# Optimization experiments

Measured on AMD Instinct MI355X. Metric: run time of the kernel, lower is better.

Reference implementation:

```python
import jax, jax.numpy as jnp
import numpy as np

NORM = float(1.0 / np.sqrt(2.0))


def haar1d_fwd(x):
    # forward 1D Haar along last axis; n must be a power of 2
    n = x.shape[-1]
    m = int(np.log2(n))
    length = n
    for _ in range(m):
        t = x[..., :length]
        e, o = t[..., ::2], t[..., 1::2]
        x = jnp.concatenate([NORM * (e + o), NORM * (e - o), x[..., length:]], axis=-1)
        length //= 2
    return x


def haar1d_inv(x):
    n = x.shape[-1]
    m = int(np.log2(n))
    length = 2
    for _ in range(m):
        half = length // 2
        a, d = x[..., :half], x[..., half:length]
        # interleave (a+d)/sqrt2 and (a-d)/sqrt2
        inter = jnp.stack([NORM * (a + d), NORM * (a - d)], axis=-1)
        inter = inter.reshape(x.shape[:-1] + (length,))
        x = jnp.concatenate([inter, x[..., length:]], axis=-1)
        length *= 2
    return x


def haar2d(x, inverse=False):
    f = haar1d_inv if inverse else haar1d_fwd
    x = f(x)                                        # along width
    x = jnp.swapaxes(f(jnp.swapaxes(x, -1, -2)), -1, -2)  # along height
    return x


def setup_inputs() -> dict:
    key = jax.random.key(0)
    k1, k2, k3, k4 = jax.random.split(key, 4)
    B, C, H, W, P = 16, 64, 256, 256, 2
    x = jax.random.normal(k1, (B, C, H, W), dtype=jnp.float32)
    v = jax.random.uniform(k2, (P, 1, 1, H, W), dtype=jnp.float32)
    conv_w = jax.random.normal(k3, (P, C, C), dtype=jnp.float32) * 0.05  # (pod, out_c, in_c)
    tau = jax.random.uniform(k4, (P, 1, 1, H, W), dtype=jnp.float32)
    return {"x": x, "v": v, "conv_w": conv_w, "tau": tau}


def reference(x, v, conv_w, tau):
    # H=W=256 are powers of 2 -> find_min_power padding is a no-op
    f1 = haar2d(x)  # forward 2D Haar
    acc = jnp.zeros_like(f1[:, :conv_w.shape[1]])
    for i in range(v.shape[0]):  # loop over pods (small, fixed)
        f3 = f1 * v[i]                                  # per-pixel spectral gate
        f4 = jnp.einsum('bchw,oc->bohw', f3, conv_w[i])  # 1x1 conv, no bias
        f5 = jnp.sign(f4) * jax.nn.relu(jnp.abs(f4) - tau[i])  # soft threshold
        acc = acc + f5
    y = haar2d(acc, inverse=True)
    return y + x  # residual
```

## Files before the change

kernel.cpp:

```cpp
#include <hip/hip_runtime.h>
#include <hip/hip_bf16.h>


namespace {

constexpr float kNorm = 0.70710678118654752440f;

typedef __attribute__((ext_vector_type(8))) short short8;
typedef __attribute__((ext_vector_type(4))) float f32x4;
typedef __attribute__((ext_vector_type(8))) unsigned short ushort8;
typedef __attribute__((ext_vector_type(4))) unsigned int uint4v;

__device__ __forceinline__ int ip2ref(int p) {
  if (p == 0) return 0;
  const int j = __builtin_ctz(p) + 1;
  return (256 >> j) + (p >> j);
}
__device__ __forceinline__ int ref2ip(int r) {
  if (r == 0) return 0;
  const int tb = 31 - __builtin_clz(r);
  const int j = 8 - tb;
  return ((r - (1 << tb)) << j) | (1 << (j - 1));
}

__device__ __forceinline__ unsigned short f2bf(float f) {
  unsigned int u = __float_as_uint(f);
  u += 0x7FFFu + ((u >> 16) & 1u);
  return (unsigned short)(u >> 16);
}
__device__ __forceinline__ float bf2f(unsigned int u) {
  return __uint_as_float((u & 0xFFFFu) << 16);
}
__device__ __forceinline__ unsigned pk2(float lo, float hi) {
  return (unsigned)f2bf(lo) | ((unsigned)f2bf(hi) << 16);
}

__device__ __forceinline__ void lift3f(const float f[8], float o[8]) {
  const float a0 = kNorm * (f[0] + f[1]), d10 = kNorm * (f[0] - f[1]);
  const float a1 = kNorm * (f[2] + f[3]), d11 = kNorm * (f[2] - f[3]);
  const float a2 = kNorm * (f[4] + f[5]), d12 = kNorm * (f[4] - f[5]);
  const float a3 = kNorm * (f[6] + f[7]), d13 = kNorm * (f[6] - f[7]);
  const float b0 = kNorm * (a0 + a1), d20 = kNorm * (a0 - a1);
  const float b1 = kNorm * (a2 + a3), d21 = kNorm * (a2 - a3);
  o[0] = kNorm * (b0 + b1);
  o[4] = kNorm * (b0 - b1);
  o[2] = d20; o[6] = d21;
  o[1] = d10; o[3] = d11; o[5] = d12; o[7] = d13;
}
__device__ __forceinline__ void ilift3f(const float f[8], float o[8]) {
  const float b0 = kNorm * (f[0] + f[4]), b1 = kNorm * (f[0] - f[4]);
  const float a0 = kNorm * (b0 + f[2]), a1 = kNorm * (b0 - f[2]);
  const float a2 = kNorm * (b1 + f[6]), a3 = kNorm * (b1 - f[6]);
  o[0] = kNorm * (a0 + f[1]); o[1] = kNorm * (a0 - f[1]);
  o[2] = kNorm * (a1 + f[3]); o[3] = kNorm * (a1 - f[3]);
  o[4] = kNorm * (a2 + f[5]); o[5] = kNorm * (a2 - f[5]);
  o[6] = kNorm * (a3 + f[7]); o[7] = kNorm * (a3 - f[7]);
}

__global__ __launch_bounds__(256) void k_prep(const float* __restrict__ cw,
                                              const float* __restrict__ vv,
                                              const float* __restrict__ tt,
                                              unsigned short* __restrict__ wb,
                                              unsigned int* __restrict__ vpk,
                                              unsigned int* __restrict__ tpk) {
  const int idx = blockIdx.x * 256 + threadIdx.x;
  if (idx < 8192) wb[idx] = f2bf(cw[idx]);
  const int w = idx >> 8;
  const int hp = idx & 255;
  const int off = (ip2ref(hp) << 8) + w;
  vpk[idx] = pk2(vv[off], vv[65536 + off]);
  tpk[idx] = pk2(tt[off], tt[65536 + off]);
}

__global__ __launch_bounds__(256) void k_fwdW(const float* __restrict__ x,
                                              unsigned short* __restrict__ xt) {
  __shared__ float tile[256][33];
  const int blk = blockIdx.x;
  const int img = blk >> 3;
  const int h0 = (blk & 7) << 5;
  const int tid = threadIdx.x;

  const float* __restrict__ src = x + ((size_t)img << 16) + ((size_t)h0 << 8);

  const int hR = tid >> 3;
  const int g = tid & 7;
#pragma unroll
  for (int it = 0; it < 4; ++it) {
    const int w0 = (g + (it << 3)) << 3;
    const float4 u = *reinterpret_cast<const float4*>(src + (hR << 8) + w0);
    const float4 v2 = *reinterpret_cast<const float4*>(src + (hR << 8) + w0 + 4);
    float f[8] = {u.x, u.y, u.z, u.w, v2.x, v2.y, v2.z, v2.w};
    float o[8];
    lift3f(f, o);
#pragma unroll
    for (int j = 0; j < 8; ++j) tile[w0 + j][hR] = o[j];
  }
  __syncthreads();

  if (tid < 128) {
    const int row = tid & 31;
    const int tq = tid >> 5;
    const int wq = tq << 6;
    float f[8], o[8];
#pragma unroll
    for (int j = 0; j < 8; ++j) f[j] = tile[wq + (j << 3)][row];
    lift3f(f, o);
#pragma unroll
    for (int j = 0; j < 8; ++j) tile[wq + (j << 3)][row] = o[j];
  }
  __syncthreads();

  if (tid < 32) {
    const float f0 = tile[0][tid], f1 = tile[64][tid];
    const float f2 = tile[128][tid], f3 = tile[192][tid];
    const float a0 = kNorm * (f0 + f1), d0 = kNorm * (f0 - f1);
    const float a1 = kNorm * (f2 + f3), d1 = kNorm * (f2 - f3);
    tile[0][tid] = kNorm * (a0 + a1);
    tile[64][tid] = d0;
    tile[128][tid] = kNorm * (a0 - a1);
    tile[192][tid] = d1;
  }
  __syncthreads();

  unsigned short* __restrict__ dst = xt + ((size_t)img << 16) + h0;
#pragma unroll
  for (int k = 0; k < 4; ++k) {
    const int idx = (k << 8) + tid;
    const int wp = idx >> 2;
    const int hseg = (idx & 3) << 3;
    const int wr = ip2ref(wp);
    ushort8 s;
#pragma unroll
    for (int j = 0; j < 8; ++j) s[j] = f2bf(tile[wp][hseg + j]);
    *reinterpret_cast<ushort8*>(dst + ((size_t)wr << 8) + hseg) = s;
  }
}

__device__ __forceinline__ int swzc(int h, int cdw) {
  return (h << 5) | ((cdw + ((h & 7) << 2) + (((h >> 3) & 3) << 3)) & 31);
}

__global__ __launch_bounds__(256, 3) void k_mid(
    unsigned short* __restrict__ ws, const unsigned short* __restrict__ wb,
    const unsigned int* __restrict__ vpk, const unsigned int* __restrict__ tpk) {
  __shared__ unsigned int t32[8192];
  __shared__ unsigned int vt[512];
  unsigned short* t16 = reinterpret_cast<unsigned short*>(t32);

  const int blk = blockIdx.x;
  const int b = blk >> 8;
  const int w = blk & 255;
  const int tid = threadIdx.x;

  unsigned short* __restrict__ base = ws + ((size_t)b << 22) + ((size_t)w << 8);

  vt[tid] = vpk[(w << 8) + tid];
  vt[256 + tid] = tpk[(w << 8) + tid];

  const int l15 = tid & 15;
  const int l4 = (tid & 63) >> 4;
  short8 Bf[4][4];
#pragma unroll
  for (int og = 0; og < 4; ++og) {
    const int o = (og << 4) + l15;
    const unsigned short* wr0 = wb + (o << 6) + (l4 << 3);
    const unsigned short* wr1 = wb + 4096 + (o << 6) + (l4 << 3);
    Bf[og][0] = *reinterpret_cast<const short8*>(wr0);
    Bf[og][1] = *reinterpret_cast<const short8*>(wr0 + 32);
    Bf[og][2] = *reinterpret_cast<const short8*>(wr1);
    Bf[og][3] = *reinterpret_cast<const short8*>(wr1 + 32);
  }

  const int cdw = tid >> 3;
  const int c0 = cdw << 1;
  const int o8 = tid & 7;
#pragma unroll
  for (int it = 0; it < 4; ++it) {
    const int h0 = (o8 << 3) + (it << 6);
    const ushort8 rA =
        *reinterpret_cast<const ushort8*>(base + ((size_t)c0 << 16) + h0);
    const ushort8 rB =
        *reinterpret_cast<const ushort8*>(base + ((size_t)(c0 + 1) << 16) + h0);
    float fa[8], fb[8], oa[8], ob[8];
#pragma unroll
    for (int j = 0; j < 8; ++j) {
      fa[j] = bf2f(rA[j]);
      fb[j] = bf2f(rB[j]);
    }
    lift3f(fa, oa);
    lift3f(fb, ob);
#pragma unroll
    for (int j = 0; j < 8; ++j) t32[swzc(h0 + j, cdw)] = pk2(oa[j], ob[j]);
  }
  __syncthreads();

  if (tid < 128) {
    const int cd = tid & 31;
    const int h0 = (tid >> 5) << 6;
    unsigned int g[8];
#pragma unroll
    for (int k = 0; k < 8; ++k) g[k] = t32[swzc(h0 + (k << 3), cd)];
    float fa[8], fb[8], oa[8], ob[8];
#pragma unroll
    for (int k = 0; k < 8; ++k) {
      fa[k] = bf2f(g[k]);
      fb[k] = bf2f(g[k] >> 16);
    }
    lift3f(fa, oa);
    lift3f(fb, ob);
#pragma unroll
    for (int k = 0; k < 8; ++k)
      t32[swzc(h0 + (k << 3), cd)] = pk2(oa[k], ob[k]);
  }
  __syncthreads();

  if (tid < 32) {
    unsigned int g[4];
#pragma unroll
    for (int k = 0; k < 4; ++k) g[k] = t32[swzc(k << 6, tid)];
    float fa[4], fb[4];
#pragma unroll
    for (int k = 0; k < 4; ++k) {
      fa[k] = bf2f(g[k]);
      fb[k] = bf2f(g[k] >> 16);
    }
    const float aa0 = kNorm * (fa[0] + fa[1]), da0 = kNorm * (fa[0] - fa[1]);
    const float aa1 = kNorm * (fa[2] + fa[3]), da1 = kNorm * (fa[2] - fa[3]);
    const float ab0 = kNorm * (fb[0] + fb[1]), db0 = kNorm * (fb[0] - fb[1]);
    const float ab1 = kNorm * (fb[2] + fb[3]), db1 = kNorm * (fb[2] - fb[3]);
    t32[swzc(0, tid)] = pk2(kNorm * (aa0 + aa1), kNorm * (ab0 + ab1));
    t32[swzc(64, tid)] = pk2(da0, db0);
    t32[swzc(128, tid)] = pk2(kNorm * (aa0 - aa1), kNorm * (ab0 - ab1));
    t32[swzc(192, tid)] = pk2(da1, db1);
  }
  __syncthreads();

  const int strip = (tid >> 6) << 6;
#pragma unroll 1
  for (int mt = 0; mt < 4; ++mt) {
    const int hh = strip + (mt << 4) + l15;
    const short8 a0 =
        *reinterpret_cast<const short8*>(&t32[swzc(hh, l4 << 2)]);
    const short8 a1 =
        *reinterpret_cast<const short8*>(&t32[swzc(hh, 16 + (l4 << 2))]);
    const int hb = strip + (mt << 4) + (l4 << 2);
    const uint4v vq = *reinterpret_cast<const uint4v*>(&vt[hb]);
    const uint4v tq = *reinterpret_cast<const uint4v*>(&vt[256 + hb]);
#pragma unroll
    for (int og = 0; og < 4; ++og) {
      const int o = (og << 4) + l15;
      f32x4 accL = {0.f, 0.f, 0.f, 0.f};
      f32x4 accH = {0.f, 0.f, 0.f, 0.f};
      accL = __builtin_amdgcn_mfma_f32_16x16x32_bf16(a0, Bf[og][0], accL, 0, 0, 0);
      accH = __builtin_amdgcn_mfma_f32_16x16x32_bf16(a0, Bf[og][2], accH, 0, 0, 0);
      accL = __builtin_amdgcn_mfma_f32_16x16x32_bf16(a1, Bf[og][1], accL, 0, 0, 0);
      accH = __builtin_amdgcn_mfma_f32_16x16x32_bf16(a1, Bf[og][3], accH, 0, 0, 0);
#pragma unroll
      for (int r = 0; r < 4; ++r) {
        const float v0 = bf2f(vq[r]), v1 = bf2f(vq[r] >> 16);
        const float t0 = bf2f(tq[r]), t1 = bf2f(tq[r] >> 16);
        const float g0 = accL[r] * v0;
        const float g1 = accH[r] * v1;
        float rr = 0.f;
        const float q0 = fabsf(g0) - t0;
        if (q0 > 0.f) rr += copysignf(q0, g0);
        const float q1 = fabsf(g1) - t1;
        if (q1 > 0.f) rr += copysignf(q1, g1);
        const int idx16 = (swzc(hb + r, o >> 1) << 1) | (o & 1);
        const float Fv = bf2f(t16[idx16]);
        t16[idx16] = f2bf(rr + Fv);
      }
    }
  }
  __syncthreads();

  if (tid < 32) {
    unsigned int g[4];
#pragma unroll
    for (int k = 0; k < 4; ++k) g[k] = t32[swzc(k << 6, tid)];
    float fa[4], fb[4];
#pragma unroll
    for (int k = 0; k < 4; ++k) {
      fa[k] = bf2f(g[k]);
      fb[k] = bf2f(g[k] >> 16);
    }
    const float ua0 = kNorm * (fa[0] + fa[2]), ua1 = kNorm * (fa[0] - fa[2]);
    const float ub0 = kNorm * (fb[0] + fb[2]), ub1 = kNorm * (fb[0] - fb[2]);
    t32[swzc(0, tid)] = pk2(kNorm * (ua0 + fa[1]), kNorm * (ub0 + fb[1]));
    t32[swzc(64, tid)] = pk2(kNorm * (ua0 - fa[1]), kNorm * (ub0 - fb[1]));
    t32[swzc(128, tid)] = pk2(kNorm * (ua1 + fa[3]), kNorm * (ub1 + fb[3]));
    t32[swzc(192, tid)] = pk2(kNorm * (ua1 - fa[3]), kNorm * (ub1 - fb[3]));
  }
  __syncthreads();

  if (tid < 128) {
    const int cd = tid & 31;
    const int h0 = (tid >> 5) << 6;
    unsigned int g[8];
#pragma unroll
    for (int k = 0; k < 8; ++k) g[k] = t32[swzc(h0 + (k << 3), cd)];
    float fa[8], fb[8], oa[8], ob[8];
#pragma unroll
    for (int k = 0; k < 8; ++k) {
      fa[k] = bf2f(g[k]);
      fb[k] = bf2f(g[k] >> 16);
    }
    ilift3f(fa, oa);
    ilift3f(fb, ob);
#pragma unroll
    for (int k = 0; k < 8; ++k)
      t32[swzc(h0 + (k << 3), cd)] = pk2(oa[k], ob[k]);
  }
  __syncthreads();

#pragma unroll
  for (int it = 0; it < 4; ++it) {
    const int h0 = (o8 << 3) + (it << 6);
    unsigned int g[8];
#pragma unroll
    for (int j = 0; j < 8; ++j) g[j] = t32[swzc(h0 + j, cdw)];
    float fa[8], fb[8], oa[8], ob[8];
#pragma unroll
    for (int j = 0; j < 8; ++j) {
      fa[j] = bf2f(g[j]);
      fb[j] = bf2f(g[j] >> 16);
    }
    ilift3f(fa, oa);
    ilift3f(fb, ob);
    ushort8 sA, sB;
#pragma unroll
    for (int j = 0; j < 8; ++j) {
      sA[j] = f2bf(oa[j]);
      sB[j] = f2bf(ob[j]);
    }
    *reinterpret_cast<ushort8*>(base + ((size_t)c0 << 16) + h0) = sA;
    *reinterpret_cast<ushort8*>(base + ((size_t)(c0 + 1) << 16) + h0) = sB;
  }
}

__global__ __launch_bounds__(256) void k_invW(const unsigned short* __restrict__ at,
                                              float* __restrict__ y) {
  __shared__ float tile[256][33];
  const int blk = blockIdx.x;
  const int img = blk >> 3;
  const int h0 = (blk & 7) << 5;
  const int tid = threadIdx.x;

  const unsigned short* __restrict__ basep = at + ((size_t)img << 16) + h0;
#pragma unroll
  for (int k = 0; k < 4; ++k) {
    const int idx = (k << 8) + tid;
    const int wp = idx >> 2;
    const int hseg = (idx & 3) << 3;
    const int wr = ip2ref(wp);
    const ushort8 rv =
        *reinterpret_cast<const ushort8*>(basep + ((size_t)wr << 8) + hseg);
#pragma unroll
    for (int j = 0; j < 8; ++j) tile[wp][hseg + j] = bf2f(rv[j]);
  }
  __syncthreads();

  if (tid < 32) {
    const float f0 = tile[0][tid], f1 = tile[64][tid];
    const float f2 = tile[128][tid], f3 = tile[192][tid];
    const float u0 = kNorm * (f0 + f2), u1 = kNorm * (f0 - f2);
    tile[0][tid] = kNorm * (u0 + f1);
    tile[64][tid] = kNorm * (u0 - f1);
    tile[128][tid] = kNorm * (u1 + f3);
    tile[192][tid] = kNorm * (u1 - f3);
  }
  __syncthreads();

  if (tid < 128) {
    const int row = tid & 31;
    const int tq = tid >> 5;
    const int wq = tq << 6;
    float f[8], o[8];
#pragma unroll
    for (int j = 0; j < 8; ++j) f[j] = tile[wq + (j << 3)][row];
    ilift3f(f, o);
#pragma unroll
    for (int j = 0; j < 8; ++j) tile[wq + (j << 3)][row] = o[j];
  }
  __syncthreads();

  const int hR = tid >> 3;
  const int g = tid & 7;
  float* __restrict__ yd = y + ((size_t)img << 16) + ((size_t)h0 << 8);
#pragma unroll
  for (int it = 0; it < 4; ++it) {
    const int w0 = (g + (it << 3)) << 3;
    float f[8], o[8];
#pragma unroll
    for (int j = 0; j < 8; ++j) f[j] = tile[w0 + j][hR];
    ilift3f(f, o);
    float4 y0 = {o[0], o[1], o[2], o[3]};
    float4 y1 = {o[4], o[5], o[6], o[7]};
    *reinterpret_cast<float4*>(yd + (hR << 8) + w0) = y0;
    *reinterpret_cast<float4*>(yd + (hR << 8) + w0 + 4) = y1;
  }
}

}

extern "C" void kernel_launch(void* const* d_in, const int* in_sizes, int n_in,
                              void* d_out, int out_size, void* d_ws, size_t ws_size,
                              hipStream_t stream) {
  (void)in_sizes; (void)n_in; (void)out_size; (void)ws_size;
  const float* x  = (const float*)d_in[0];
  const float* vv = (const float*)d_in[1];
  const float* cw = (const float*)d_in[2];
  const float* tt = (const float*)d_in[3];
  float* y = (float*)d_out;
  unsigned short* ws = (unsigned short*)d_ws;
  unsigned short* wb = ws + ((size_t)64 << 20);
  unsigned int* vpk = (unsigned int*)(ws + ((size_t)64 << 20) + 16384);
  unsigned int* tpk = vpk + 65536;

  k_prep<<<256, 256, 0, stream>>>(cw, vv, tt, wb, vpk, tpk);
  k_fwdW<<<8192, 256, 0, stream>>>(x, ws);
  k_mid <<<4096, 256, 0, stream>>>(ws, wb, vpk, tpk);
  k_invW<<<8192, 256, 0, stream>>>(ws, y);
}
```

Before: 261.6 us.

## Pack row pairs as bf16x2 in LDS for width Haar transforms

Reworks the forward and inverse width-direction Haar kernels so each LDS word holds two adjacent rows packed as bf16 pairs. The 256x33 fp32 tile becomes a 16x260 uint tile, so the transpose moves half as many bytes and uses vectorized 16-byte LDS accesses and rotated index orders to spread banks. This cuts LDS traffic and shared-memory footprint, which may allow more resident blocks. In exchange, intermediate lifting stages are rounded to bf16 inside the kernel instead of only at the output, which adds precision loss.

```diff
diff --git a/kernel.cpp b/kernel.cpp
--- a/kernel.cpp
+++ b/kernel.cpp
@@ -74,51 +74,80 @@
 
 __global__ __launch_bounds__(256) void k_fwdW(const float* __restrict__ x,
                                               unsigned short* __restrict__ xt) {
-  __shared__ float tile[256][33];
+  __shared__ unsigned int t[16][260];
   const int blk = blockIdx.x;
   const int img = blk >> 3;
   const int h0 = (blk & 7) << 5;
   const int tid = threadIdx.x;
 
   const float* __restrict__ src = x + ((size_t)img << 16) + ((size_t)h0 << 8);
-
-  const int hR = tid >> 3;
   const int g = tid & 7;
-#pragma unroll
-  for (int it = 0; it < 4; ++it) {
-    const int w0 = (g + (it << 3)) << 3;
-    const float4 u = *reinterpret_cast<const float4*>(src + (hR << 8) + w0);
-    const float4 v2 = *reinterpret_cast<const float4*>(src + (hR << 8) + w0 + 4);
-    float f[8] = {u.x, u.y, u.z, u.w, v2.x, v2.y, v2.z, v2.w};
-    float o[8];
-    lift3f(f, o);
-#pragma unroll
-    for (int j = 0; j < 8; ++j) tile[w0 + j][hR] = o[j];
-  }
-  __syncthreads();
-
-  if (tid < 128) {
-    const int row = tid & 31;
-    const int tq = tid >> 5;
-    const int wq = tq << 6;
-    float f[8], o[8];
-#pragma unroll
-    for (int j = 0; j < 8; ++j) f[j] = tile[wq + (j << 3)][row];
-    lift3f(f, o);
-#pragma unroll
-    for (int j = 0; j < 8; ++j) tile[wq + (j << 3)][row] = o[j];
-  }
-  __syncthreads();
-
-  if (tid < 32) {
-    const float f0 = tile[0][tid], f1 = tile[64][tid];
-    const float f2 = tile[128][tid], f3 = tile[192][tid];
-    const float a0 = kNorm * (f0 + f1), d0 = kNorm * (f0 - f1);
-    const float a1 = kNorm * (f2 + f3), d1 = kNorm * (f2 - f3);
-    tile[0][tid] = kNorm * (a0 + a1);
-    tile[64][tid] = d0;
-    tile[128][tid] = kNorm * (a0 - a1);
-    tile[192][tid] = d1;
+  const int hd = (tid >> 3) & 15;
+  const int half = tid >> 7;
+
+  const float* __restrict__ r0 = src + (hd << 9);
+  const float* __restrict__ r1 = r0 + 256;
+#pragma unroll
+  for (int it = 0; it < 2; ++it) {
+    const int w0 = (g + (half << 3) + (it << 4)) << 3;
+    const float4 a0 = *reinterpret_cast<const float4*>(r0 + w0);
+    const float4 a1 = *reinterpret_cast<const float4*>(r0 + w0 + 4);
+    const float4 b0 = *reinterpret_cast<const float4*>(r1 + w0);
+    const float4 b1 = *reinterpret_cast<const float4*>(r1 + w0 + 4);
+    float fe[8] = {a0.x, a0.y, a0.z, a0.w, a1.x, a1.y, a1.z, a1.w};
+    float fo[8] = {b0.x, b0.y, b0.z, b0.w, b1.x, b1.y, b1.z, b1.w};
+    float oe[8], oo[8];
+    lift3f(fe, oe);
+    lift3f(fo, oo);
+    uint4v q0 = {pk2(oe[0], oo[0]), pk2(oe[1], oo[1]),
+                 pk2(oe[2], oo[2]), pk2(oe[3], oo[3])};
+    uint4v q1 = {pk2(oe[4], oo[4]), pk2(oe[5], oo[5]),
+                 pk2(oe[6], oo[6]), pk2(oe[7], oo[7])};
+    *reinterpret_cast<uint4v*>(&t[hd][w0]) = q0;
+    *reinterpret_cast<uint4v*>(&t[hd][w0 + 4]) = q1;
+  }
+  __syncthreads();
+
+  if (tid < 64) {
+    const int hd2 = tid & 15;
+    const int q = tid >> 4;
+    const int wq = q << 6;
+    unsigned gd[8];
+#pragma unroll
+    for (int k0 = 0; k0 < 8; ++k0) {
+      const int k = (k0 + (q << 1)) & 7;
+      gd[k] = t[hd2][wq + (k << 3)];
+    }
+    float fe[8], fo[8], oe[8], oo[8];
+#pragma unroll
+    for (int k = 0; k < 8; ++k) {
+      fe[k] = bf2f(gd[k]);
+      fo[k] = bf2f(gd[k] >> 16);
+    }
+    lift3f(fe, oe);
+    lift3f(fo, oo);
+#pragma unroll
+    for (int k0 = 0; k0 < 8; ++k0) {
+      const int k = (k0 + (q << 1)) & 7;
+      t[hd2][wq + (k << 3)] = pk2(oe[k], oo[k]);
+    }
+  }
+  __syncthreads();
+
+  if (tid < 16) {
+    const unsigned d0 = t[tid][0], d1 = t[tid][64];
+    const unsigned d2 = t[tid][128], d3 = t[tid][192];
+    const float e0 = bf2f(d0), e1 = bf2f(d1), e2 = bf2f(d2), e3 = bf2f(d3);
+    const float p0 = bf2f(d0 >> 16), p1 = bf2f(d1 >> 16);
+    const float p2 = bf2f(d2 >> 16), p3 = bf2f(d3 >> 16);
+    const float ae0 = kNorm * (e0 + e1), de0 = kNorm * (e0 - e1);
+    const float ae1 = kNorm * (e2 + e3), de1 = kNorm * (e2 - e3);
+    const float ao0 = kNorm * (p0 + p1), do0 = kNorm * (p0 - p1);
+    const float ao1 = kNorm * (p2 + p3), do1 = kNorm * (p2 - p3);
+    t[tid][0] = pk2(kNorm * (ae0 + ae1), kNorm * (ao0 + ao1));
+    t[tid][64] = pk2(de0, do0);
+    t[tid][128] = pk2(kNorm * (ae0 - ae1), kNorm * (ao0 - ao1));
+    t[tid][192] = pk2(de1, do1);
   }
   __syncthreads();
 
@@ -127,12 +156,10 @@
   for (int k = 0; k < 4; ++k) {
     const int idx = (k << 8) + tid;
     const int wp = idx >> 2;
-    const int hseg = (idx & 3) << 3;
+    const int hq = (idx & 3) << 2;
     const int wr = ip2ref(wp);
-    ushort8 s;
-#pragma unroll
-    for (int j = 0; j < 8; ++j) s[j] = f2bf(tile[wp][hseg + j]);
-    *reinterpret_cast<ushort8*>(dst + ((size_t)wr << 8) + hseg) = s;
+    uint4v qv = {t[hq][wp], t[hq + 1][wp], t[hq + 2][wp], t[hq + 3][wp]};
+    *reinterpret_cast<uint4v*>(dst + ((size_t)wr << 8) + (hq << 1)) = qv;
   }
 }
 
@@ -340,7 +367,7 @@
 
 __global__ __launch_bounds__(256) void k_invW(const unsigned short* __restrict__ at,
                                               float* __restrict__ y) {
-  __shared__ float tile[256][33];
+  __shared__ unsigned int t[16][260];
   const int blk = blockIdx.x;
   const int img = blk >> 3;
   const int h0 = (blk & 7) << 5;
@@ -351,53 +378,87 @@
   for (int k = 0; k < 4; ++k) {
     const int idx = (k << 8) + tid;
     const int wp = idx >> 2;
-    const int hseg = (idx & 3) << 3;
+    const int hq = (idx & 3) << 2;
     const int wr = ip2ref(wp);
-    const ushort8 rv =
-        *reinterpret_cast<const ushort8*>(basep + ((size_t)wr << 8) + hseg);
-#pragma unroll
-    for (int j = 0; j < 8; ++j) tile[wp][hseg + j] = bf2f(rv[j]);
-  }
-  __syncthreads();
-
-  if (tid < 32) {
-    const float f0 = tile[0][tid], f1 = tile[64][tid];
-    const float f2 = tile[128][tid], f3 = tile[192][tid];
-    const float u0 = kNorm * (f0 + f2), u1 = kNorm * (f0 - f2);
-    tile[0][tid] = kNorm * (u0 + f1);
-    tile[64][tid] = kNorm * (u0 - f1);
-    tile[128][tid] = kNorm * (u1 + f3);
-    tile[192][tid] = kNorm * (u1 - f3);
-  }
-  __syncthreads();
-
-  if (tid < 128) {
-    const int row = tid & 31;
-    const int tq = tid >> 5;
-    const int wq = tq << 6;
-    float f[8], o[8];
-#pragma unroll
-    for (int j = 0; j < 8; ++j) f[j] = tile[wq + (j << 3)][row];
-    ilift3f(f, o);
-#pragma unroll
-    for (int j = 0; j < 8; ++j) tile[wq + (j << 3)][row] = o[j];
-  }
-  __syncthreads();
-
-  const int hR = tid >> 3;
+    const uint4v qv = *reinterpret_cast<const uint4v*>(
+        basep + ((size_t)wr << 8) + (hq << 1));
+    t[hq][wp] = qv[0];
+    t[hq + 1][wp] = qv[1];
+    t[hq + 2][wp] = qv[2];
+    t[hq + 3][wp] = qv[3];
+  }
+  __syncthreads();
+
+  if (tid < 16) {
+    const unsigned d0 = t[tid][0], d1 = t[tid][64];
+    const unsigned d2 = t[tid][128], d3 = t[tid][192];
+    const float e0 = bf2f(d0), e1 = bf2f(d1), e2 = bf2f(d2), e3 = bf2f(d3);
+    const float p0 = bf2f(d0 >> 16), p1 = bf2f(d1 >> 16);
+    const float p2 = bf2f(d2 >> 16), p3 = bf2f(d3 >> 16);
+    const float ue0 = kNorm * (e0 + e2), ue1 = kNorm * (e0 - e2);
+    const float uo0 = kNorm * (p0 + p2), uo1 = kNorm * (p0 - p2);
+    t[tid][0] = pk2(kNorm * (ue0 + e1), kNorm * (uo0 + p1));
+    t[tid][64] = pk2(kNorm * (ue0 - e1), kNorm * (uo0 - p1));
+    t[tid][128] = pk2(kNorm * (ue1 + e3), kNorm * (uo1 + p3));
+    t[tid][192] = pk2(kNorm * (ue1 - e3), kNorm * (uo1 - p3));
+  }
+  __syncthreads();
+
+  if (tid < 64) {
+    const int hd2 = tid & 15;
+    const int q = tid >> 4;
+    const int wq = q << 6;
+    unsigned gd[8];
+#pragma unroll
+    for (int k0 = 0; k0 < 8; ++k0) {
+      const int k = (k0 + (q << 1)) & 7;
+      gd[k] = t[hd2][wq + (k << 3)];
+    }
+    float fe[8], fo[8], oe[8], oo[8];
+#pragma unroll
+    for (int k = 0; k < 8; ++k) {
+      fe[k] = bf2f(gd[k]);
+      fo[k] = bf2f(gd[k] >> 16);
+    }
+    ilift3f(fe, oe);
+    ilift3f(fo, oo);
+#pragma unroll
+    for (int k0 = 0; k0 < 8; ++k0) {
+      const int k = (k0 + (q << 1)) & 7;
+      t[hd2][wq + (k << 3)] = pk2(oe[k], oo[k]);
+    }
+  }
+  __syncthreads();
+
   const int g = tid & 7;
-  float* __restrict__ yd = y + ((size_t)img << 16) + ((size_t)h0 << 8);
-#pragma unroll
-  for (int it = 0; it < 4; ++it) {
-    const int w0 = (g + (it << 3)) << 3;
-    float f[8], o[8];
-#pragma unroll
-    for (int j = 0; j < 8; ++j) f[j] = tile[w0 + j][hR];
-    ilift3f(f, o);
-    float4 y0 = {o[0], o[1], o[2], o[3]};
-    float4 y1 = {o[4], o[5], o[6], o[7]};
-    *reinterpret_cast<float4*>(yd + (hR << 8) + w0) = y0;
-    *reinterpret_cast<float4*>(yd + (hR << 8) + w0 + 4) = y1;
+  const int hd = (tid >> 3) & 15;
+  const int half = tid >> 7;
+  float* __restrict__ yr0 =
+      y + ((size_t)img << 16) + ((size_t)h0 << 8) + (hd << 9);
+  float* __restrict__ yr1 = yr0 + 256;
+#pragma unroll
+  for (int it = 0; it < 2; ++it) {
+    const int w0 = (g + (half << 3) + (it << 4)) << 3;
+    const uint4v qa = *reinterpret_cast<const uint4v*>(&t[hd][w0]);
+    const uint4v qb = *reinterpret_cast<const uint4v*>(&t[hd][w0 + 4]);
+    float fe[8], fo[8], oe[8], oo[8];
+#pragma unroll
+    for (int j = 0; j < 4; ++j) {
+      fe[j] = bf2f(qa[j]);
+      fo[j] = bf2f(qa[j] >> 16);
+      fe[4 + j] = bf2f(qb[j]);
+      fo[4 + j] = bf2f(qb[j] >> 16);
+    }
+    ilift3f(fe, oe);
+    ilift3f(fo, oo);
+    float4 ya0 = {oe[0], oe[1], oe[2], oe[3]};
+    float4 ya1 = {oe[4], oe[5], oe[6], oe[7]};
+    float4 yb0 = {oo[0], oo[1], oo[2], oo[3]};
+    float4 yb1 = {oo[4], oo[5], oo[6], oo[7]};
+    *reinterpret_cast<float4*>(yr0 + w0) = ya0;
+    *reinterpret_cast<float4*>(yr0 + w0 + 4) = ya1;
+    *reinterpret_cast<float4*>(yr1 + w0) = yb0;
+    *reinterpret_cast<float4*>(yr1 + w0 + 4) = yb1;
   }
 }
 
```

New measurement: 262.6 us (median of 2 runs). Within noise of the previous version (+0.4%).
